# Optimization experiments

Hardware: AMD Instinct MI355X
Metric: run time of the kernel (lower is better)

The kernel has to match this reference:

```python
import jax, jax.numpy as jnp
import numpy as np

N, E, R, D = 50000, 800000, 8, 64
BN_EPS = 1e-5


def _bn_relu(x, g, b):
    # training-mode BatchNorm1d (biased variance) + relu
    m = x.mean(axis=0)
    v = x.var(axis=0)
    return jax.nn.relu((x - m) / jnp.sqrt(v + BN_EPS) * g + b)


def setup_inputs() -> dict:
    key = jax.random.key(0)
    ks = jax.random.split(key, 10)
    return {
        'x': jax.random.normal(ks[0], (N, D), dtype=jnp.float32),
        'edge_weight': jax.random.uniform(ks[1], (E,), dtype=jnp.float32),
        'W_lin1': jax.random.normal(ks[2], (D, R * D), dtype=jnp.float32) * 0.05,
        'b_lin1': jnp.zeros((D,), jnp.float32),
        'W_self1': jax.random.normal(ks[3], (D, D), dtype=jnp.float32) * 0.05,
        'b_self1': jnp.zeros((D,), jnp.float32),
        'gamma1': jnp.ones((D,), jnp.float32),
        'beta1': jnp.zeros((D,), jnp.float32),
        'W_lin2': jax.random.normal(ks[4], (D, D), dtype=jnp.float32) * 0.05,
        'b_lin2': jnp.zeros((D,), jnp.float32),
        'W_self2': jax.random.normal(ks[5], (D, D), dtype=jnp.float32) * 0.05,
        'b_self2': jnp.zeros((D,), jnp.float32),
        'gamma2': jnp.ones((D,), jnp.float32),
        'beta2': jnp.zeros((D,), jnp.float32),
        'node_in': jax.random.randint(ks[6], (E,), 0, N, dtype=jnp.int32),
        'node_out': jax.random.randint(ks[7], (E,), 0, N, dtype=jnp.int32),
        'relation': jax.random.randint(ks[8], (E,), 0, R, dtype=jnp.int32),
        'num_relation': R,
    }


def reference(x, edge_weight, W_lin1, b_lin1, W_self1, b_self1, gamma1, beta1,
              W_lin2, b_lin2, W_self2, b_self2, gamma2, beta2,
              node_in, node_out, relation, num_relation):
    Nn, Din = x.shape
    Rr = int(num_relation)
    seg = node_out * Rr + relation  # node_out * num_relation + relation
    # degree normalization of edge weights (shared by both layers)
    deg = jax.ops.segment_sum(edge_weight, seg, num_segments=Nn * Rr)
    ew = edge_weight / deg[seg]

    # layer 1: relationalGraphConv
    msgs = x[node_in] * ew[:, None]  # [E, D]
    upd = jax.ops.segment_sum(msgs, seg, num_segments=Nn * Rr)
    upd = upd.reshape(Nn, Rr * Din)  # node-major flatten, matches torch .view
    h = upd @ W_lin1.T + b_lin1 + x @ W_self1.T + b_self1
    h = _bn_relu(h, gamma1, beta1)  # [N, D]

    # layer 2: relationalGraph (per-relation outputs)
    msgs2 = h[node_in] * ew[:, None]
    upd2 = jax.ops.segment_sum(msgs2, seg, num_segments=Nn * Rr)  # [N*R, D] node-major
    upd2 = upd2.reshape(Nn, Rr, -1).transpose(1, 0, 2).reshape(Rr * Nn, -1)  # relation-major
    h_rep = jnp.tile(h, (Rr, 1))  # input.repeat(R, 1)
    out = upd2 @ W_lin2.T + b_lin2 + h_rep @ W_self2.T + b_self2
    out = _bn_relu(out, gamma2, beta2)
    return out.reshape(Rr, Nn, -1)
```

## Files before the change

### kernel.cpp

```cpp
#include <hip/hip_runtime.h>


#define GATHER_GRID 2048
#define SCAN_CHUNK 4096
#define RED_BLOCKS 64
#define ZERO_BLOCKS 256
#define PACK_BLOCKS 16
#define COUNT_BLOCKS 2048
#define PLACE_BLOCKS 1024

typedef short bf16x8 __attribute__((ext_vector_type(8)));
typedef float f32x4 __attribute__((ext_vector_type(4)));

static __device__ __forceinline__ float bf2f(unsigned short u) {
  return __uint_as_float(((unsigned)u) << 16);
}
static __device__ __forceinline__ unsigned short f2bf(float f) {
  unsigned u = __float_as_uint(f);
  u += 0x7FFFu + ((u >> 16) & 1u);
  return (unsigned short)(u >> 16);
}

__global__ void k_zeropack(int* __restrict__ cnt, int NR, int R,
                           const float* __restrict__ Wlin1, const float* __restrict__ Wself1,
                           const float* __restrict__ Wlin2, const float* __restrict__ Wself2,
                           unsigned short* __restrict__ wb1, unsigned short* __restrict__ wb2) {
  if (blockIdx.x < ZERO_BLOCKS) {
    int i = blockIdx.x * 256 + threadIdx.x;
    int stride = ZERO_BLOCKS * 256;
    for (int k = i; k < NR; k += stride) cnt[k] = 0;
  } else {
    int i = (blockIdx.x - ZERO_BLOCKS) * 256 + threadIdx.x;
    int stride = PACK_BLOCKS * 256;
    int n1 = (R + 1) * 64 * 64;
    int n2 = 2 * 64 * 64;
    for (int k = i; k < n1 + n2; k += stride) {
      if (k < n1) {
        int r = k >> 6, d = k & 63;
        float v;
        if (r < R * 64) {
          int s = r >> 6, j = r & 63;
          v = Wlin1[j * (R * 64) + s * 64 + d];
        } else {
          v = Wself1[(r - R * 64) * 64 + d];
        }
        wb1[k] = f2bf(v);
      } else {
        int k2 = k - n1;
        int r = k2 >> 6, d = k2 & 63;
        float v = (r < 64) ? Wlin2[r * 64 + d] : Wself2[(r - 64) * 64 + d];
        wb2[k2] = f2bf(v);
      }
    }
  }
}

__global__ __launch_bounds__(256) void k_countgemm(
    const int* __restrict__ node_out, const int* __restrict__ rel,
    int* __restrict__ cnt, int* __restrict__ tmp, int E, int R,
    const float* __restrict__ xf, int M, const unsigned short* __restrict__ Wb,
    unsigned short* __restrict__ outLinB, unsigned short* __restrict__ outSelf,
    int mblocks) {
  if ((int)blockIdx.x < mblocks) {
    int m0 = blockIdx.x * 64;
    int wid = threadIdx.x >> 6;
    int lane = threadIdx.x & 63;
    int mrow = m0 + wid * 16 + (lane & 15);
    int mload = (mrow < M) ? mrow : (M - 1);
    const float* arow = xf + (size_t)mload * 64 + 8 * (lane >> 4);
    float4 af0 = *(const float4*)(arow);
    float4 af1 = *(const float4*)(arow + 4);
    float4 af2 = *(const float4*)(arow + 32);
    float4 af3 = *(const float4*)(arow + 36);
    bf16x8 a0, a1;
    a0[0] = (short)f2bf(af0.x); a0[1] = (short)f2bf(af0.y);
    a0[2] = (short)f2bf(af0.z); a0[3] = (short)f2bf(af0.w);
    a0[4] = (short)f2bf(af1.x); a0[5] = (short)f2bf(af1.y);
    a0[6] = (short)f2bf(af1.z); a0[7] = (short)f2bf(af1.w);
    a1[0] = (short)f2bf(af2.x); a1[1] = (short)f2bf(af2.y);
    a1[2] = (short)f2bf(af2.z); a1[3] = (short)f2bf(af2.w);
    a1[4] = (short)f2bf(af3.x); a1[5] = (short)f2bf(af3.y);
    a1[6] = (short)f2bf(af3.z); a1[7] = (short)f2bf(af3.w);
    int rbase = m0 + wid * 16 + ((lane >> 4) << 2);
    int cbase = lane & 15;
    for (int slab = 0; slab <= R; ++slab) {
      const unsigned short* wrow = Wb + ((size_t)slab * 64 + (lane & 15)) * 64 + 8 * (lane >> 4);
      unsigned short* op = (slab < R) ? (outLinB + (size_t)slab * M * 64) : outSelf;
      #pragma unroll
      for (int nt = 0; nt < 4; ++nt) {
        bf16x8 b0 = *(const bf16x8*)(wrow + nt * 16 * 64);
        bf16x8 b1 = *(const bf16x8*)(wrow + nt * 16 * 64 + 32);
        f32x4 c = {};
        c = __builtin_amdgcn_mfma_f32_16x16x32_bf16(a0, b0, c, 0, 0, 0);
        c = __builtin_amdgcn_mfma_f32_16x16x32_bf16(a1, b1, c, 0, 0, 0);
        int col = nt * 16 + cbase;
        #pragma unroll
        for (int rg = 0; rg < 4; ++rg) {
          int grow = rbase + rg;
          if (grow < M) op[(size_t)grow * 64 + col] = f2bf(c[rg]);
        }
      }
    }
  } else {
    int i = ((int)blockIdx.x - mblocks) * 256 + threadIdx.x;
    int stride = COUNT_BLOCKS * 256;
    for (int e = i; e < E; e += stride) {
      int seg = node_out[e] * R + rel[e];
      tmp[e] = atomicAdd(&cnt[seg], 1);
    }
  }
}

__global__ __launch_bounds__(256) void k_scan1(const int* __restrict__ cnt,
                                               int* __restrict__ bsum, int NR) {
  __shared__ int red[256];
  int tid = threadIdx.x;
  int base = blockIdx.x * SCAN_CHUNK;
  int s = 0;
  for (int i = tid; i < SCAN_CHUNK; i += 256) {
    int idx = base + i;
    if (idx < NR) s += cnt[idx];
  }
  red[tid] = s;
  __syncthreads();
  for (int off = 128; off > 0; off >>= 1) {
    if (tid < off) red[tid] += red[tid + off];
    __syncthreads();
  }
  if (tid == 0) bsum[blockIdx.x] = red[0];
}

__global__ void k_scan2(const int* __restrict__ bsum, int* __restrict__ bpre,
                        int* __restrict__ rowptr_end, int NB) {
  int lane = threadIdx.x;
  int carry = 0;
  for (int base = 0; base < NB; base += 64) {
    int i = base + lane;
    int v = (i < NB) ? bsum[i] : 0;
    int incl = v;
    #pragma unroll
    for (int off = 1; off < 64; off <<= 1) {
      int u = __shfl_up(incl, off);
      if (lane >= off) incl += u;
    }
    if (i < NB) bpre[i] = carry + incl - v;
    carry += __shfl(incl, 63);
  }
  if (lane == 0) *rowptr_end = carry;
}

__global__ __launch_bounds__(256) void k_scan3(const int* __restrict__ cnt,
                                               const int* __restrict__ bpre,
                                               int* __restrict__ rowptr,
                                               unsigned* __restrict__ descT,
                                               int NR, int R, int Nn) {
  __shared__ int wtot[4];
  int tid = threadIdx.x, lane = tid & 63, wid = tid >> 6;
  int base = blockIdx.x * SCAN_CHUNK + tid * 16;
  int v[16];
  int t = 0;
  #pragma unroll
  for (int i = 0; i < 16; i++) {
    int idx = base + i;
    v[i] = (idx < NR) ? cnt[idx] : 0;
    t += v[i];
  }
  int incl = t;
  #pragma unroll
  for (int off = 1; off < 64; off <<= 1) {
    int u = __shfl_up(incl, off);
    if (lane >= off) incl += u;
  }
  if (lane == 63) wtot[wid] = incl;
  __syncthreads();
  int woff = 0;
  for (int w = 0; w < wid; w++) woff += wtot[w];
  int start = bpre[blockIdx.x] + woff + incl - t;
  #pragma unroll
  for (int i = 0; i < 16; i++) {
    int idx = base + i;
    if (idx < NR) {
      rowptr[idx] = start;
      int n = (int)((unsigned)idx / (unsigned)R);
      int r = idx - n * R;
      descT[(size_t)r * Nn + n] = (unsigned)start | ((unsigned)v[i] << 20);
    }
    start += v[i];
  }
}

__global__ void k_place(const float* __restrict__ w, const int* __restrict__ node_out,
                        const int* __restrict__ node_in, const int* __restrict__ rel,
                        const int* __restrict__ rowptr, const int* __restrict__ tmp,
                        unsigned* __restrict__ ep4, int E, int R) {
  int i = blockIdx.x * blockDim.x + threadIdx.x;
  int stride = gridDim.x * blockDim.x;
  for (int e = i; e < E; e += stride) {
    int seg = node_out[e] * R + rel[e];
    int pos = rowptr[seg] + tmp[e];
    ep4[pos] = (unsigned)node_in[e] | ((unsigned)f2bf(w[e]) << 16);
  }
}

__global__ __launch_bounds__(256) void k_gather1(
    const int* __restrict__ rowptr, const unsigned* __restrict__ ep4,
    const unsigned short* __restrict__ y1, const unsigned short* __restrict__ s1,
    unsigned short* __restrict__ h_pre, float* __restrict__ part, int N, int R) {
  int lane = threadIdx.x & 63;
  int wid = threadIdx.x >> 6;
  int l16 = lane & 15;
  int lg = lane >> 4;
  int c0 = l16 * 4;
  int grp = blockIdx.x * 16 + wid * 4 + lg;
  int ngrp = gridDim.x * 16;
  float lsum[4] = {0.f, 0.f, 0.f, 0.f}, lsq[4] = {0.f, 0.f, 0.f, 0.f};
  for (int n = grp; n < N; n += ngrp) {
    int segbase = n * R;
    int k = rowptr[segbase];
    float t0 = 0.f, t1 = 0.f, t2 = 0.f, t3 = 0.f;
    for (int r = 0; r < R; r++) {
      int k1 = rowptr[segbase + r + 1];
      if (k < k1) {
        const unsigned short* yb = y1 + (size_t)r * N * 64;
        float a0 = 0.f, a1 = 0.f, a2 = 0.f, a3 = 0.f, d = 0.f;
        for (; k + 1 < k1; k += 2) {
          unsigned pA = ep4[k], pB = ep4[k + 1];
          ushort4 uA = *(const ushort4*)&yb[(size_t)(pA & 0xFFFFu) * 64 + c0];
          ushort4 uB = *(const ushort4*)&yb[(size_t)(pB & 0xFFFFu) * 64 + c0];
          float wA = bf2f((unsigned short)(pA >> 16));
          float wB = bf2f((unsigned short)(pB >> 16));
          d += wA + wB;
          a0 = fmaf(wA, bf2f(uA.x), a0); a1 = fmaf(wA, bf2f(uA.y), a1);
          a2 = fmaf(wA, bf2f(uA.z), a2); a3 = fmaf(wA, bf2f(uA.w), a3);
          a0 = fmaf(wB, bf2f(uB.x), a0); a1 = fmaf(wB, bf2f(uB.y), a1);
          a2 = fmaf(wB, bf2f(uB.z), a2); a3 = fmaf(wB, bf2f(uB.w), a3);
        }
        if (k < k1) {
          unsigned p = ep4[k];
          float w = bf2f((unsigned short)(p >> 16));
          ushort4 u = *(const ushort4*)&yb[(size_t)(p & 0xFFFFu) * 64 + c0];
          d += w;
          a0 = fmaf(w, bf2f(u.x), a0); a1 = fmaf(w, bf2f(u.y), a1);
          a2 = fmaf(w, bf2f(u.z), a2); a3 = fmaf(w, bf2f(u.w), a3);
        }
        if (d != 0.f) {
          float inv = 1.f / d;
          t0 = fmaf(a0, inv, t0); t1 = fmaf(a1, inv, t1);
          t2 = fmaf(a2, inv, t2); t3 = fmaf(a3, inv, t3);
        }
        k = k1;
      }
    }
    ushort4 su = *(const ushort4*)&s1[(size_t)n * 64 + c0];
    float v0 = t0 + bf2f(su.x), v1 = t1 + bf2f(su.y);
    float v2 = t2 + bf2f(su.z), v3 = t3 + bf2f(su.w);
    ushort4 o; o.x = f2bf(v0); o.y = f2bf(v1); o.z = f2bf(v2); o.w = f2bf(v3);
    *(ushort4*)&h_pre[(size_t)n * 64 + c0] = o;
    lsum[0] += v0; lsq[0] += v0 * v0;
    lsum[1] += v1; lsq[1] += v1 * v1;
    lsum[2] += v2; lsq[2] += v2 * v2;
    lsum[3] += v3; lsq[3] += v3 * v3;
  }
  __shared__ float sp[16][64], sq[16][64];
  int g = wid * 4 + lg;
  #pragma unroll
  for (int i = 0; i < 4; i++) { sp[g][c0 + i] = lsum[i]; sq[g][c0 + i] = lsq[i]; }
  __syncthreads();
  if (threadIdx.x < 64) {
    int j = threadIdx.x;
    float s = 0.f, q = 0.f;
    #pragma unroll
    for (int gg = 0; gg < 16; gg++) { s += sp[gg][j]; q += sq[gg][j]; }
    part[(size_t)blockIdx.x * 128 + j] = s;
    part[(size_t)blockIdx.x * 128 + 64 + j] = q;
  }
}

__global__ __launch_bounds__(256) void k_gemm2bn(
    const unsigned short* __restrict__ hp, int M,
    const unsigned short* __restrict__ Wb, int nslab,
    const float* __restrict__ ss,
    unsigned short* __restrict__ outLinB, unsigned short* __restrict__ outSelf) {
  __shared__ float sss[128];
  if (threadIdx.x < 128) sss[threadIdx.x] = ss[threadIdx.x];
  __syncthreads();
  int m0 = blockIdx.x * 64;
  int wid = threadIdx.x >> 6;
  int lane = threadIdx.x & 63;
  int mrow = m0 + wid * 16 + (lane & 15);
  int mload = (mrow < M) ? mrow : (M - 1);
  int cb = 8 * (lane >> 4);
  const unsigned short* arow = hp + (size_t)mload * 64 + cb;
  ushort4 u0 = *(const ushort4*)(arow);
  ushort4 u1 = *(const ushort4*)(arow + 4);
  ushort4 u2 = *(const ushort4*)(arow + 32);
  ushort4 u3 = *(const ushort4*)(arow + 36);
  bf16x8 a0, a1;
  #pragma unroll
  for (int j = 0; j < 4; j++) {
    unsigned short uu0 = (&u0.x)[j], uu1 = (&u1.x)[j], uu2 = (&u2.x)[j], uu3 = (&u3.x)[j];
    a0[j]     = (short)f2bf(fmaxf(fmaf(bf2f(uu0), sss[cb + j],      sss[64 + cb + j]), 0.f));
    a0[j + 4] = (short)f2bf(fmaxf(fmaf(bf2f(uu1), sss[cb + 4 + j],  sss[64 + cb + 4 + j]), 0.f));
    a1[j]     = (short)f2bf(fmaxf(fmaf(bf2f(uu2), sss[cb + 32 + j], sss[64 + cb + 32 + j]), 0.f));
    a1[j + 4] = (short)f2bf(fmaxf(fmaf(bf2f(uu3), sss[cb + 36 + j], sss[64 + cb + 36 + j]), 0.f));
  }
  int rbase = m0 + wid * 16 + ((lane >> 4) << 2);
  int cbase = lane & 15;
  for (int slab = 0; slab <= nslab; ++slab) {
    const unsigned short* wrow = Wb + ((size_t)slab * 64 + (lane & 15)) * 64 + 8 * (lane >> 4);
    unsigned short* op = (slab < nslab) ? (outLinB + (size_t)slab * M * 64) : outSelf;
    #pragma unroll
    for (int nt = 0; nt < 4; ++nt) {
      bf16x8 b0 = *(const bf16x8*)(wrow + nt * 16 * 64);
      bf16x8 b1 = *(const bf16x8*)(wrow + nt * 16 * 64 + 32);
      f32x4 c = {};
      c = __builtin_amdgcn_mfma_f32_16x16x32_bf16(a0, b0, c, 0, 0, 0);
      c = __builtin_amdgcn_mfma_f32_16x16x32_bf16(a1, b1, c, 0, 0, 0);
      int col = nt * 16 + cbase;
      #pragma unroll
      for (int rg = 0; rg < 4; ++rg) {
        int grow = rbase + rg;
        if (grow < M) op[(size_t)grow * 64 + col] = f2bf(c[rg]);
      }
    }
  }
}

__global__ __launch_bounds__(256) void k_gather2_statsave(
    const unsigned* __restrict__ descT, const unsigned* __restrict__ ep4,
    const unsigned short* __restrict__ z, const unsigned short* __restrict__ s2,
    float* __restrict__ part, unsigned short* __restrict__ pre, int N, int R) {
  int lane = threadIdx.x & 63;
  int wid = threadIdx.x >> 6;
  int l16 = lane & 15;
  int lg = lane >> 4;
  int c0 = l16 * 4;
  int grp = blockIdx.x * 16 + wid * 4 + lg;
  int ngrp = gridDim.x * 16;
  int NR = N * R;
  float lsum[4] = {0.f, 0.f, 0.f, 0.f}, lsq[4] = {0.f, 0.f, 0.f, 0.f};
  for (int s = grp; s < NR; s += ngrp) {
    unsigned r = (unsigned)s / (unsigned)N;
    int n = s - (int)r * N;
    unsigned desc = descT[s];
    int k = (int)(desc & 0xFFFFFu);
    int cnt = (int)(desc >> 20);
    int k1 = k + cnt;
    float a0 = 0.f, a1 = 0.f, a2 = 0.f, a3 = 0.f, d = 0.f;
    for (; k + 1 < k1; k += 2) {
      unsigned pA = ep4[k], pB = ep4[k + 1];
      ushort4 uA = *(const ushort4*)&z[(size_t)(pA & 0xFFFFu) * 64 + c0];
      ushort4 uB = *(const ushort4*)&z[(size_t)(pB & 0xFFFFu) * 64 + c0];
      float wA = bf2f((unsigned short)(pA >> 16));
      float wB = bf2f((unsigned short)(pB >> 16));
      d += wA + wB;
      a0 = fmaf(wA, bf2f(uA.x), a0); a1 = fmaf(wA, bf2f(uA.y), a1);
      a2 = fmaf(wA, bf2f(uA.z), a2); a3 = fmaf(wA, bf2f(uA.w), a3);
      a0 = fmaf(wB, bf2f(uB.x), a0); a1 = fmaf(wB, bf2f(uB.y), a1);
      a2 = fmaf(wB, bf2f(uB.z), a2); a3 = fmaf(wB, bf2f(uB.w), a3);
    }
    if (k < k1) {
      unsigned p = ep4[k];
      float w = bf2f((unsigned short)(p >> 16));
      ushort4 u = *(const ushort4*)&z[(size_t)(p & 0xFFFFu) * 64 + c0];
      d += w;
      a0 = fmaf(w, bf2f(u.x), a0); a1 = fmaf(w, bf2f(u.y), a1);
      a2 = fmaf(w, bf2f(u.z), a2); a3 = fmaf(w, bf2f(u.w), a3);
    }
    if (d != 0.f) {
      float inv = 1.f / d;
      a0 *= inv; a1 *= inv; a2 *= inv; a3 *= inv;
    }
    ushort4 su = *(const ushort4*)&s2[(size_t)n * 64 + c0];
    float v0 = a0 + bf2f(su.x), v1 = a1 + bf2f(su.y);
    float v2 = a2 + bf2f(su.z), v3 = a3 + bf2f(su.w);
    ushort4 o; o.x = f2bf(v0); o.y = f2bf(v1); o.z = f2bf(v2); o.w = f2bf(v3);
    *(ushort4*)&pre[(size_t)s * 128 + c0] = o;
    lsum[0] += v0; lsq[0] += v0 * v0;
    lsum[1] += v1; lsq[1] += v1 * v1;
    lsum[2] += v2; lsq[2] += v2 * v2;
    lsum[3] += v3; lsq[3] += v3 * v3;
  }
  __shared__ float sp[16][64], sq[16][64];
  int g = wid * 4 + lg;
  #pragma unroll
  for (int i = 0; i < 4; i++) { sp[g][c0 + i] = lsum[i]; sq[g][c0 + i] = lsq[i]; }
  __syncthreads();
  if (threadIdx.x < 64) {
    int j = threadIdx.x;
    float s = 0.f, q = 0.f;
    #pragma unroll
    for (int gg = 0; gg < 16; gg++) { s += sp[gg][j]; q += sq[gg][j]; }
    part[(size_t)blockIdx.x * 128 + j] = s;
    part[(size_t)blockIdx.x * 128 + 64 + j] = q;
  }
}

__global__ __launch_bounds__(256) void k_bnrelu_inplace(
    float* __restrict__ out, const float* __restrict__ ss, int NR) {
  __shared__ float sss[128];
  if (threadIdx.x < 128) sss[threadIdx.x] = ss[threadIdx.x];
  __syncthreads();
  int l16 = threadIdx.x & 15;
  int c0 = l16 * 4;
  float sc0 = sss[c0], sc1 = sss[c0 + 1], sc2 = sss[c0 + 2], sc3 = sss[c0 + 3];
  float sh0 = sss[64 + c0], sh1 = sss[64 + c0 + 1], sh2 = sss[64 + c0 + 2], sh3 = sss[64 + c0 + 3];
  int row = blockIdx.x * 16 + (threadIdx.x >> 4);
  int stride = gridDim.x * 16;
  const unsigned short* pre = (const unsigned short*)out;
  for (int s = row; s < NR; s += stride) {
    ushort4 u = *(const ushort4*)&pre[(size_t)s * 128 + c0];
    float v0 = fmaxf(fmaf(bf2f(u.x), sc0, sh0), 0.f);
    float v1 = fmaxf(fmaf(bf2f(u.y), sc1, sh1), 0.f);
    float v2 = fmaxf(fmaf(bf2f(u.z), sc2, sh2), 0.f);
    float v3 = fmaxf(fmaf(bf2f(u.w), sc3, sh3), 0.f);
    *(float4*)&out[(size_t)s * 64 + c0] = make_float4(v0, v1, v2, v3);
  }
}

__global__ __launch_bounds__(256) void k_red1(const float* __restrict__ part,
                                              float* __restrict__ part2, int P) {
  int j = threadIdx.x & 127;
  int g = threadIdx.x >> 7;
  int rows = (P + RED_BLOCKS - 1) / RED_BLOCKS;
  int base = blockIdx.x * rows;
  float acc = 0.f;
  for (int i = g; i < rows; i += 2) {
    int idx = base + i;
    if (idx < P) acc += part[(size_t)idx * 128 + j];
  }
  __shared__ float red[2][128];
  red[g][j] = acc;
  __syncthreads();
  if (threadIdx.x < 128) part2[(size_t)blockIdx.x * 128 + j] = red[0][j] + red[1][j];
}

__global__ __launch_bounds__(1024) void k_bnstats(
    const float* __restrict__ part, int P, float M,
    const float* __restrict__ gamma, const float* __restrict__ beta,
    float* __restrict__ ss) {
  __shared__ float red[1024];
  int tid = threadIdx.x;
  int j = tid & 127;
  int g = tid >> 7;
  float acc = 0.f;
  for (int i = g; i < P; i += 8) acc += part[(size_t)i * 128 + j];
  red[tid] = acc;
  __syncthreads();
  if (tid < 128) {
    float s = 0.f;
    for (int gg = 0; gg < 8; gg++) s += red[gg * 128 + tid];
    red[tid] = s;
  }
  __syncthreads();
  if (tid < 64) {
    float s = red[tid], q = red[64 + tid];
    float mean = s / M;
    float var = q / M - mean * mean;
    float sc = gamma[tid] / sqrtf(var + 1e-5f);
    ss[tid] = sc;
    ss[64 + tid] = beta[tid] - mean * sc;
  }
}

extern "C" void kernel_launch(void* const* d_in, const int* in_sizes, int n_in,
                              void* d_out, int out_size, void* d_ws, size_t ws_size,
                              hipStream_t stream) {
  const float* x        = (const float*)d_in[0];
  const float* edge_w   = (const float*)d_in[1];
  const float* W_lin1   = (const float*)d_in[2];
  const float* W_self1  = (const float*)d_in[4];
  const float* gamma1   = (const float*)d_in[6];
  const float* beta1    = (const float*)d_in[7];
  const float* W_lin2   = (const float*)d_in[8];
  const float* W_self2  = (const float*)d_in[10];
  const float* gamma2   = (const float*)d_in[12];
  const float* beta2    = (const float*)d_in[13];
  const int* node_in    = (const int*)d_in[14];
  const int* node_out   = (const int*)d_in[15];
  const int* relation   = (const int*)d_in[16];

  int N = in_sizes[0] / 64;
  int E = in_sizes[1];
  int R = in_sizes[2] / (64 * 64);
  int NR = N * R;
  int NB = (NR + SCAN_CHUNK - 1) / SCAN_CHUNK;

  char* p = (char*)d_ws;
  auto alloc = [&](size_t bytes) { char* r = p; p += (bytes + 255) & ~(size_t)255; return r; };
  int* cnt      = (int*)alloc(4ull * NR);
  int* rowptr   = (int*)alloc(4ull * (NR + 1));
  unsigned* descT = (unsigned*)alloc(4ull * NR);
  int* tmp      = (int*)alloc(4ull * E);
  int* bsum     = (int*)alloc(4ull * NB);
  int* bpre     = (int*)alloc(4ull * NB);
  unsigned* ep4 = (unsigned*)alloc(4ull * E);
  unsigned short* wb1 = (unsigned short*)alloc(2ull * (R + 1) * 64 * 64);
  unsigned short* wb2 = (unsigned short*)alloc(2ull * 2 * 64 * 64);
  unsigned short* s1    = (unsigned short*)alloc(2ull * N * 64);
  unsigned short* h_pre = (unsigned short*)alloc(2ull * N * 64);
  unsigned short* z     = (unsigned short*)alloc(2ull * N * 64);
  unsigned short* s2    = (unsigned short*)alloc(2ull * N * 64);
  float* part   = (float*)alloc(4ull * GATHER_GRID * 128);
  float* part2  = (float*)alloc(4ull * RED_BLOCKS * 128);
  float* ss1    = (float*)alloc(4ull * 128);
  float* ss2    = (float*)alloc(4ull * 128);

  unsigned short* y1 = (unsigned short*)d_out;

  int mblocks = (N + 63) / 64;

  k_zeropack<<<ZERO_BLOCKS + PACK_BLOCKS, 256, 0, stream>>>(
      cnt, NR, R, W_lin1, W_self1, W_lin2, W_self2, wb1, wb2);
  k_countgemm<<<mblocks + COUNT_BLOCKS, 256, 0, stream>>>(
      node_out, relation, cnt, tmp, E, R, x, N, wb1, y1, s1, mblocks);
  k_scan1<<<NB, 256, 0, stream>>>(cnt, bsum, NR);
  k_scan2<<<1, 64, 0, stream>>>(bsum, bpre, &rowptr[NR], NB);
  k_scan3<<<NB, 256, 0, stream>>>(cnt, bpre, rowptr, descT, NR, R, N);
  k_place<<<PLACE_BLOCKS, 256, 0, stream>>>(
      edge_w, node_out, node_in, relation, rowptr, tmp, ep4, E, R);

  k_gather1<<<GATHER_GRID, 256, 0, stream>>>(rowptr, ep4, y1, s1, h_pre, part, N, R);
  k_red1<<<RED_BLOCKS, 256, 0, stream>>>(part, part2, GATHER_GRID);
  k_bnstats<<<1, 1024, 0, stream>>>(part2, RED_BLOCKS, (float)N, gamma1, beta1, ss1);

  k_gemm2bn<<<mblocks, 256, 0, stream>>>(h_pre, N, wb2, 1, ss1, z, s2);
  k_gather2_statsave<<<GATHER_GRID, 256, 0, stream>>>(
      descT, ep4, z, s2, part, (unsigned short*)d_out, N, R);
  k_red1<<<RED_BLOCKS, 256, 0, stream>>>(part, part2, GATHER_GRID);
  k_bnstats<<<1, 1024, 0, stream>>>(part2, RED_BLOCKS, (float)N * R, gamma2, beta2, ss2);
  k_bnrelu_inplace<<<4096, 256, 0, stream>>>((float*)d_out, ss2, NR);
}
```

Before: 239.4 us.

## Reorder layer-1 to aggregate raw features first, then apply one fused GEMM

Layer 1 no longer projects x through every relation slab before gathering. It converts x to bf16, gathers and normalises neighbour features per relation into an N×512 buffer, then runs a single K=576 MFMA GEMM that also folds in the self term and emits BN partial statistics. This removes the R-fold projection GEMM and its writes of R×N×64 outputs. In exchange it adds a write and read of the N×512 aggregation buffer and a separate kernel launch, and it rounds the aggregated values to bf16 before the GEMM.

Measured after the change: 256.7 us. 7.3% more time.

```diff
diff --git a/kernel.cpp b/kernel.cpp
--- a/kernel.cpp
+++ b/kernel.cpp
@@ -6,6 +6,7 @@
 #define RED_BLOCKS 64
 #define ZERO_BLOCKS 256
 #define PACK_BLOCKS 16
+#define XB_BLOCKS 64
 #define COUNT_BLOCKS 2048
 #define PLACE_BLOCKS 1024
 
@@ -32,77 +33,38 @@
   } else {
     int i = (blockIdx.x - ZERO_BLOCKS) * 256 + threadIdx.x;
     int stride = PACK_BLOCKS * 256;
-    int n1 = (R + 1) * 64 * 64;
+    int KW = R * 64 + 64;
+    int n1 = 64 * KW;
     int n2 = 2 * 64 * 64;
-    for (int k = i; k < n1 + n2; k += stride) {
-      if (k < n1) {
-        int r = k >> 6, d = k & 63;
-        float v;
-        if (r < R * 64) {
-          int s = r >> 6, j = r & 63;
-          v = Wlin1[j * (R * 64) + s * 64 + d];
-        } else {
-          v = Wself1[(r - R * 64) * 64 + d];
-        }
-        wb1[k] = f2bf(v);
+    for (int t = i; t < n1 + n2; t += stride) {
+      if (t < n1) {
+        int j = t / KW, k = t - j * KW;
+        float v = (k < R * 64) ? Wlin1[j * (R * 64) + k] : Wself1[j * 64 + (k - R * 64)];
+        wb1[t] = f2bf(v);
       } else {
-        int k2 = k - n1;
-        int r = k2 >> 6, d = k2 & 63;
+        int t2 = t - n1;
+        int r = t2 >> 6, d = t2 & 63;
         float v = (r < 64) ? Wlin2[r * 64 + d] : Wself2[(r - 64) * 64 + d];
-        wb2[k2] = f2bf(v);
+        wb2[t2] = f2bf(v);
       }
     }
   }
 }
 
-__global__ __launch_bounds__(256) void k_countgemm(
-    const int* __restrict__ node_out, const int* __restrict__ rel,
-    int* __restrict__ cnt, int* __restrict__ tmp, int E, int R,
-    const float* __restrict__ xf, int M, const unsigned short* __restrict__ Wb,
-    unsigned short* __restrict__ outLinB, unsigned short* __restrict__ outSelf,
-    int mblocks) {
-  if ((int)blockIdx.x < mblocks) {
-    int m0 = blockIdx.x * 64;
-    int wid = threadIdx.x >> 6;
-    int lane = threadIdx.x & 63;
-    int mrow = m0 + wid * 16 + (lane & 15);
-    int mload = (mrow < M) ? mrow : (M - 1);
-    const float* arow = xf + (size_t)mload * 64 + 8 * (lane >> 4);
-    float4 af0 = *(const float4*)(arow);
-    float4 af1 = *(const float4*)(arow + 4);
-    float4 af2 = *(const float4*)(arow + 32);
-    float4 af3 = *(const float4*)(arow + 36);
-    bf16x8 a0, a1;
-    a0[0] = (short)f2bf(af0.x); a0[1] = (short)f2bf(af0.y);
-    a0[2] = (short)f2bf(af0.z); a0[3] = (short)f2bf(af0.w);
-    a0[4] = (short)f2bf(af1.x); a0[5] = (short)f2bf(af1.y);
-    a0[6] = (short)f2bf(af1.z); a0[7] = (short)f2bf(af1.w);
-    a1[0] = (short)f2bf(af2.x); a1[1] = (short)f2bf(af2.y);
-    a1[2] = (short)f2bf(af2.z); a1[3] = (short)f2bf(af2.w);
-    a1[4] = (short)f2bf(af3.x); a1[5] = (short)f2bf(af3.y);
-    a1[6] = (short)f2bf(af3.z); a1[7] = (short)f2bf(af3.w);
-    int rbase = m0 + wid * 16 + ((lane >> 4) << 2);
-    int cbase = lane & 15;
-    for (int slab = 0; slab <= R; ++slab) {
-      const unsigned short* wrow = Wb + ((size_t)slab * 64 + (lane & 15)) * 64 + 8 * (lane >> 4);
-      unsigned short* op = (slab < R) ? (outLinB + (size_t)slab * M * 64) : outSelf;
-      #pragma unroll
-      for (int nt = 0; nt < 4; ++nt) {
-        bf16x8 b0 = *(const bf16x8*)(wrow + nt * 16 * 64);
-        bf16x8 b1 = *(const bf16x8*)(wrow + nt * 16 * 64 + 32);
-        f32x4 c = {};
-        c = __builtin_amdgcn_mfma_f32_16x16x32_bf16(a0, b0, c, 0, 0, 0);
-        c = __builtin_amdgcn_mfma_f32_16x16x32_bf16(a1, b1, c, 0, 0, 0);
-        int col = nt * 16 + cbase;
-        #pragma unroll
-        for (int rg = 0; rg < 4; ++rg) {
-          int grow = rbase + rg;
-          if (grow < M) op[(size_t)grow * 64 + col] = f2bf(c[rg]);
-        }
-      }
+__global__ void k_countx(const int* __restrict__ node_out, const int* __restrict__ rel,
+                         int* __restrict__ cnt, int* __restrict__ tmp, int E, int R,
+                         const float4* __restrict__ xin, ushort4* __restrict__ xb, int n4) {
+  if (blockIdx.x < XB_BLOCKS) {
+    int i = blockIdx.x * 256 + threadIdx.x;
+    int stride = XB_BLOCKS * 256;
+    for (int k = i; k < n4; k += stride) {
+      float4 v = xin[k];
+      ushort4 o;
+      o.x = f2bf(v.x); o.y = f2bf(v.y); o.z = f2bf(v.z); o.w = f2bf(v.w);
+      xb[k] = o;
     }
   } else {
-    int i = ((int)blockIdx.x - mblocks) * 256 + threadIdx.x;
+    int i = (blockIdx.x - XB_BLOCKS) * 256 + threadIdx.x;
     int stride = COUNT_BLOCKS * 256;
     for (int e = i; e < E; e += stride) {
       int seg = node_out[e] * R + rel[e];
@@ -202,10 +164,10 @@
   }
 }
 
-__global__ __launch_bounds__(256) void k_gather1(
+__global__ __launch_bounds__(256) void k_gatherx(
     const int* __restrict__ rowptr, const unsigned* __restrict__ ep4,
-    const unsigned short* __restrict__ y1, const unsigned short* __restrict__ s1,
-    unsigned short* __restrict__ h_pre, float* __restrict__ part, int N, int R) {
+    const unsigned short* __restrict__ xb, unsigned short* __restrict__ updx,
+    int N, int R) {
   int lane = threadIdx.x & 63;
   int wid = threadIdx.x >> 6;
   int l16 = lane & 15;
@@ -213,64 +175,107 @@
   int c0 = l16 * 4;
   int grp = blockIdx.x * 16 + wid * 4 + lg;
   int ngrp = gridDim.x * 16;
-  float lsum[4] = {0.f, 0.f, 0.f, 0.f}, lsq[4] = {0.f, 0.f, 0.f, 0.f};
   for (int n = grp; n < N; n += ngrp) {
     int segbase = n * R;
     int k = rowptr[segbase];
-    float t0 = 0.f, t1 = 0.f, t2 = 0.f, t3 = 0.f;
     for (int r = 0; r < R; r++) {
       int k1 = rowptr[segbase + r + 1];
+      float a0 = 0.f, a1 = 0.f, a2 = 0.f, a3 = 0.f, d = 0.f;
+      for (; k + 1 < k1; k += 2) {
+        unsigned pA = ep4[k], pB = ep4[k + 1];
+        ushort4 uA = *(const ushort4*)&xb[(size_t)(pA & 0xFFFFu) * 64 + c0];
+        ushort4 uB = *(const ushort4*)&xb[(size_t)(pB & 0xFFFFu) * 64 + c0];
+        float wA = bf2f((unsigned short)(pA >> 16));
+        float wB = bf2f((unsigned short)(pB >> 16));
+        d += wA + wB;
+        a0 = fmaf(wA, bf2f(uA.x), a0); a1 = fmaf(wA, bf2f(uA.y), a1);
+        a2 = fmaf(wA, bf2f(uA.z), a2); a3 = fmaf(wA, bf2f(uA.w), a3);
+        a0 = fmaf(wB, bf2f(uB.x), a0); a1 = fmaf(wB, bf2f(uB.y), a1);
+        a2 = fmaf(wB, bf2f(uB.z), a2); a3 = fmaf(wB, bf2f(uB.w), a3);
+      }
       if (k < k1) {
-        const unsigned short* yb = y1 + (size_t)r * N * 64;
-        float a0 = 0.f, a1 = 0.f, a2 = 0.f, a3 = 0.f, d = 0.f;
-        for (; k + 1 < k1; k += 2) {
-          unsigned pA = ep4[k], pB = ep4[k + 1];
-          ushort4 uA = *(const ushort4*)&yb[(size_t)(pA & 0xFFFFu) * 64 + c0];
-          ushort4 uB = *(const ushort4*)&yb[(size_t)(pB & 0xFFFFu) * 64 + c0];
-          float wA = bf2f((unsigned short)(pA >> 16));
-          float wB = bf2f((unsigned short)(pB >> 16));
-          d += wA + wB;
-          a0 = fmaf(wA, bf2f(uA.x), a0); a1 = fmaf(wA, bf2f(uA.y), a1);
-          a2 = fmaf(wA, bf2f(uA.z), a2); a3 = fmaf(wA, bf2f(uA.w), a3);
-          a0 = fmaf(wB, bf2f(uB.x), a0); a1 = fmaf(wB, bf2f(uB.y), a1);
-          a2 = fmaf(wB, bf2f(uB.z), a2); a3 = fmaf(wB, bf2f(uB.w), a3);
-        }
-        if (k < k1) {
-          unsigned p = ep4[k];
-          float w = bf2f((unsigned short)(p >> 16));
-          ushort4 u = *(const ushort4*)&yb[(size_t)(p & 0xFFFFu) * 64 + c0];
-          d += w;
-          a0 = fmaf(w, bf2f(u.x), a0); a1 = fmaf(w, bf2f(u.y), a1);
-          a2 = fmaf(w, bf2f(u.z), a2); a3 = fmaf(w, bf2f(u.w), a3);
-        }
-        if (d != 0.f) {
-          float inv = 1.f / d;
-          t0 = fmaf(a0, inv, t0); t1 = fmaf(a1, inv, t1);
-          t2 = fmaf(a2, inv, t2); t3 = fmaf(a3, inv, t3);
-        }
+        unsigned p = ep4[k];
+        float w = bf2f((unsigned short)(p >> 16));
+        ushort4 u = *(const ushort4*)&xb[(size_t)(p & 0xFFFFu) * 64 + c0];
+        d += w;
+        a0 = fmaf(w, bf2f(u.x), a0); a1 = fmaf(w, bf2f(u.y), a1);
+        a2 = fmaf(w, bf2f(u.z), a2); a3 = fmaf(w, bf2f(u.w), a3);
         k = k1;
       }
-    }
-    ushort4 su = *(const ushort4*)&s1[(size_t)n * 64 + c0];
-    float v0 = t0 + bf2f(su.x), v1 = t1 + bf2f(su.y);
-    float v2 = t2 + bf2f(su.z), v3 = t3 + bf2f(su.w);
-    ushort4 o; o.x = f2bf(v0); o.y = f2bf(v1); o.z = f2bf(v2); o.w = f2bf(v3);
-    *(ushort4*)&h_pre[(size_t)n * 64 + c0] = o;
-    lsum[0] += v0; lsq[0] += v0 * v0;
-    lsum[1] += v1; lsq[1] += v1 * v1;
-    lsum[2] += v2; lsq[2] += v2 * v2;
-    lsum[3] += v3; lsq[3] += v3 * v3;
+      if (d != 0.f) {
+        float inv = 1.f / d;
+        a0 *= inv; a1 *= inv; a2 *= inv; a3 *= inv;
+      }
+      ushort4 o; o.x = f2bf(a0); o.y = f2bf(a1); o.z = f2bf(a2); o.w = f2bf(a3);
+      *(ushort4*)&updx[(size_t)n * 512 + r * 64 + c0] = o;
+    }
+  }
+}
+
+__global__ __launch_bounds__(256) void k_gemm1b(
+    const unsigned short* __restrict__ updx, const unsigned short* __restrict__ xb,
+    int M, const unsigned short* __restrict__ wb1, unsigned short* __restrict__ h_pre,
+    float* __restrict__ part) {
+  int m0 = blockIdx.x * 64;
+  int wid = threadIdx.x >> 6;
+  int lane = threadIdx.x & 63;
+  int mrow = m0 + wid * 16 + (lane & 15);
+  int mload = (mrow < M) ? mrow : (M - 1);
+  int koff = 8 * (lane >> 4);
+  const unsigned short* aU = updx + (size_t)mload * 512 + koff;
+  const unsigned short* aX = xb + (size_t)mload * 64 + koff;
+  const unsigned short* wr = wb1 + (size_t)(lane & 15) * 576 + koff;
+  f32x4 acc[4] = {{0,0,0,0},{0,0,0,0},{0,0,0,0},{0,0,0,0}};
+  #pragma unroll
+  for (int kk = 0; kk < 16; ++kk) {
+    bf16x8 a = *(const bf16x8*)(aU + kk * 32);
+    #pragma unroll
+    for (int nt = 0; nt < 4; ++nt) {
+      bf16x8 b = *(const bf16x8*)(wr + (size_t)nt * 16 * 576 + kk * 32);
+      acc[nt] = __builtin_amdgcn_mfma_f32_16x16x32_bf16(a, b, acc[nt], 0, 0, 0);
+    }
+  }
+  #pragma unroll
+  for (int kk = 0; kk < 2; ++kk) {
+    bf16x8 a = *(const bf16x8*)(aX + kk * 32);
+    #pragma unroll
+    for (int nt = 0; nt < 4; ++nt) {
+      bf16x8 b = *(const bf16x8*)(wr + (size_t)nt * 16 * 576 + 512 + kk * 32);
+      acc[nt] = __builtin_amdgcn_mfma_f32_16x16x32_bf16(a, b, acc[nt], 0, 0, 0);
+    }
+  }
+  int rbase = m0 + wid * 16 + ((lane >> 4) << 2);
+  int cbase = lane & 15;
+  #pragma unroll
+  for (int nt = 0; nt < 4; ++nt) {
+    int col = nt * 16 + cbase;
+    #pragma unroll
+    for (int rg = 0; rg < 4; ++rg) {
+      int grow = rbase + rg;
+      if (grow < M) h_pre[(size_t)grow * 64 + col] = f2bf(acc[nt][rg]);
+    }
   }
   __shared__ float sp[16][64], sq[16][64];
-  int g = wid * 4 + lg;
-  #pragma unroll
-  for (int i = 0; i < 4; i++) { sp[g][c0 + i] = lsum[i]; sq[g][c0 + i] = lsq[i]; }
+  int strip = wid * 4 + (lane >> 4);
+  #pragma unroll
+  for (int nt = 0; nt < 4; ++nt) {
+    float cs = 0.f, cq = 0.f;
+    #pragma unroll
+    for (int rg = 0; rg < 4; ++rg) {
+      int grow = rbase + rg;
+      float v = (grow < M) ? acc[nt][rg] : 0.f;
+      cs += v; cq += v * v;
+    }
+    int col = nt * 16 + cbase;
+    sp[strip][col] = cs;
+    sq[strip][col] = cq;
+  }
   __syncthreads();
   if (threadIdx.x < 64) {
     int j = threadIdx.x;
     float s = 0.f, q = 0.f;
     #pragma unroll
-    for (int gg = 0; gg < 16; gg++) { s += sp[gg][j]; q += sq[gg][j]; }
+    for (int g = 0; g < 16; g++) { s += sp[g][j]; q += sq[g][j]; }
     part[(size_t)blockIdx.x * 128 + j] = s;
     part[(size_t)blockIdx.x * 128 + 64 + j] = q;
   }
@@ -495,9 +500,8 @@
   int* bsum     = (int*)alloc(4ull * NB);
   int* bpre     = (int*)alloc(4ull * NB);
   unsigned* ep4 = (unsigned*)alloc(4ull * E);
-  unsigned short* wb1 = (unsigned short*)alloc(2ull * (R + 1) * 64 * 64);
+  unsigned short* wb1 = (unsigned short*)alloc(2ull * 64 * (R * 64 + 64));
   unsigned short* wb2 = (unsigned short*)alloc(2ull * 2 * 64 * 64);
-  unsigned short* s1    = (unsigned short*)alloc(2ull * N * 64);
   unsigned short* h_pre = (unsigned short*)alloc(2ull * N * 64);
   unsigned short* z     = (unsigned short*)alloc(2ull * N * 64);
   unsigned short* s2    = (unsigned short*)alloc(2ull * N * 64);
@@ -506,22 +510,24 @@
   float* ss1    = (float*)alloc(4ull * 128);
   float* ss2    = (float*)alloc(4ull * 128);
 
-  unsigned short* y1 = (unsigned short*)d_out;
+  unsigned short* updx = (unsigned short*)d_out;
+  unsigned short* xb   = updx + (size_t)N * 512;
 
   int mblocks = (N + 63) / 64;
 
   k_zeropack<<<ZERO_BLOCKS + PACK_BLOCKS, 256, 0, stream>>>(
       cnt, NR, R, W_lin1, W_self1, W_lin2, W_self2, wb1, wb2);
-  k_countgemm<<<mblocks + COUNT_BLOCKS, 256, 0, stream>>>(
-      node_out, relation, cnt, tmp, E, R, x, N, wb1, y1, s1, mblocks);
+  k_countx<<<XB_BLOCKS + COUNT_BLOCKS, 256, 0, stream>>>(
+      node_out, relation, cnt, tmp, E, R, (const float4*)x, (ushort4*)xb, N * 64 / 4);
   k_scan1<<<NB, 256, 0, stream>>>(cnt, bsum, NR);
   k_scan2<<<1, 64, 0, stream>>>(bsum, bpre, &rowptr[NR], NB);
   k_scan3<<<NB, 256, 0, stream>>>(cnt, bpre, rowptr, descT, NR, R, N);
   k_place<<<PLACE_BLOCKS, 256, 0, stream>>>(
       edge_w, node_out, node_in, relation, rowptr, tmp, ep4, E, R);
 
-  k_gather1<<<GATHER_GRID, 256, 0, stream>>>(rowptr, ep4, y1, s1, h_pre, part, N, R);
-  k_red1<<<RED_BLOCKS, 256, 0, stream>>>(part, part2, GATHER_GRID);
+  k_gatherx<<<GATHER_GRID, 256, 0, stream>>>(rowptr, ep4, xb, updx, N, R);
+  k_gemm1b<<<mblocks, 256, 0, stream>>>(updx, xb, N, wb1, h_pre, part);
+  k_red1<<<RED_BLOCKS, 256, 0, stream>>>(part, part2, mblocks);
   k_bnstats<<<1, 1024, 0, stream>>>(part2, RED_BLOCKS, (float)N, gamma1, beta1, ss1);
 
   k_gemm2bn<<<mblocks, 256, 0, stream>>>(h_pre, N, wb2, 1, ss1, z, s2);
```
